# Performance work log

Hardware: AMD Instinct MI355X
Metric: run time of the kernel (lower is better)

The kernel has to match this reference:

```python
import jax, jax.numpy as jnp
import numpy as np

NUM_NODES = 100000
FEAT_DIM = 256
H1 = 256
H2 = 256
NUM_CLASSES = 64
B = 4096
F1 = 25
F2 = 10


def setup_inputs() -> dict:
    key = jax.random.key(0)
    k0, k1, k2, ke, kw1, kw2, kw3 = jax.random.split(key, 7)
    T0 = jax.random.randint(k0, (B,), 0, NUM_NODES)
    T1 = jax.random.randint(k1, (B, F1), 0, NUM_NODES)
    T2 = jax.random.randint(k2, (B * F1, F2), 0, NUM_NODES)
    emb = jax.random.normal(ke, (NUM_NODES, FEAT_DIM), dtype=jnp.float32)
    # nn.Linear(in, out, bias=False) stores weight as [out, in]
    W1 = jax.random.normal(kw1, (H1, 2 * FEAT_DIM), dtype=jnp.float32) * (1.0 / np.sqrt(2 * FEAT_DIM))
    W2 = jax.random.normal(kw2, (H2, 2 * H1), dtype=jnp.float32) * (1.0 / np.sqrt(2 * H1))
    W3 = jax.random.normal(kw3, (NUM_CLASSES, H2), dtype=jnp.float32) * (1.0 / np.sqrt(H2))
    return {"T0": T0, "T1": T1, "T2": T2, "emb": emb, "W1": W1, "W2": W2, "W3": W3}


def reference(T0, T1, T2, emb, W1, W2, W3):
    # hop-0 roots: [B, D]; hop-1 neighbor mean: [B, D]
    feat_0 = emb[T0]
    x = emb[T1].mean(axis=1)
    h0 = jax.nn.relu(jnp.concatenate([feat_0, x], axis=1) @ W1.T)  # [B, H1]
    # dropout is identity in eval mode (p applied only in training)
    # hop-1 nodes with hop-2 neighbor mean: [B*F1, D] each
    feat_1 = emb[T1].reshape(-1, FEAT_DIM)
    x2 = emb[T2].mean(axis=1)  # [B*F1, D]
    h1 = jax.nn.relu(jnp.concatenate([feat_1, x2], axis=1) @ W1.T)  # [B*F1, H1]
    h1 = h1.reshape(B, F1, H1).mean(axis=1)  # [B, H1]
    combined = jnp.concatenate([h0, h1], axis=1)  # [B, 2*H1]
    embedding = jax.nn.relu(combined @ W2.T)  # [B, H2]
    scores = embedding @ W3.T  # [B, C]
    return scores
```

## Files before the change

kernel.cpp:

```cpp
#include <hip/hip_runtime.h>
#include <hip/hip_bf16.h>


typedef __bf16  bf16x8 __attribute__((ext_vector_type(8)));
typedef __bf16  bf16x4 __attribute__((ext_vector_type(4)));
typedef float   f32x4  __attribute__((ext_vector_type(4)));
typedef float   f32x2  __attribute__((ext_vector_type(2)));

#define BATCH     4096
#define F1        25
#define F2        10
#define NNODES    100000
#define ZY_NT     3125
#define ZY_BLOCKS 512

__device__ __forceinline__ uint2 pack4_bf16(float a, float b, float c, float d) {
    union { __bf16 h[4]; uint2 u; } p;
    p.h[0] = (__bf16)a; p.h[1] = (__bf16)b; p.h[2] = (__bf16)c; p.h[3] = (__bf16)d;
    return p.u;
}

__global__ __launch_bounds__(256) void prep_weights(const float* __restrict__ W1,
                                                    const float* __restrict__ W2,
                                                    const float* __restrict__ W3,
                                                    __bf16* __restrict__ Wzy,
                                                    __bf16* __restrict__ W2b,
                                                    __bf16* __restrict__ W3b) {
    int blk = blockIdx.x;
    if (blk < 64) {
        int i = blk * 256 + threadIdx.x;
        int r  = i >> 5;
        int c0 = (i & 31) * 8;
        const float* src = (r < 256) ? (W1 + (size_t)r * 512 + c0)
                                     : (W1 + (size_t)(r - 256) * 512 + 256 + c0);
        float4 a = reinterpret_cast<const float4*>(src)[0];
        float4 b = reinterpret_cast<const float4*>(src)[1];
        uint4 o;
        uint2 pa = pack4_bf16(a.x, a.y, a.z, a.w);
        uint2 pb = pack4_bf16(b.x, b.y, b.z, b.w);
        o.x = pa.x; o.y = pa.y; o.z = pb.x; o.w = pb.y;
        *reinterpret_cast<uint4*>(Wzy + (size_t)r * 256 + c0) = o;
    } else {
        const float* in; __bf16* out;
        int i;
        if (blk < 128) { in = W2; out = W2b; i = (blk - 64) * 256 + threadIdx.x; }
        else           { in = W3; out = W3b; i = (blk - 128) * 256 + threadIdx.x; }
        float4 v0 = reinterpret_cast<const float4*>(in)[i * 2];
        float4 v1 = reinterpret_cast<const float4*>(in)[i * 2 + 1];
        uint4 o;
        uint2 a = pack4_bf16(v0.x, v0.y, v0.z, v0.w);
        uint2 b = pack4_bf16(v1.x, v1.y, v1.z, v1.w);
        o.x = a.x; o.y = a.y; o.z = b.x; o.w = b.y;
        reinterpret_cast<uint4*>(out)[i] = o;
    }
}

__global__ __launch_bounds__(512, 2) void gemm_ZY(const float* __restrict__ emb,
                                                  const __bf16* __restrict__ Wzy,
                                                  __bf16* __restrict__ Ztab,
                                                  unsigned char* __restrict__ Y8) {
    __shared__ __align__(16) char Abuf[2][16384];
    __shared__ __align__(16) __bf16 Ybuf[8][32][72];
    const int tid  = threadIdx.x;
    const int wid  = tid >> 6;
    const int lane = tid & 63;
    const int lr   = lane & 15;
    const int kg   = lane >> 4;
    const int n0   = wid * 64;

    bf16x8 wfrag[4][8];
    {
        const __bf16* Wb = Wzy + (size_t)(n0 + lr) * 256 + kg * 8;
#pragma unroll
        for (int ni = 0; ni < 4; ++ni)
#pragma unroll
            for (int kt = 0; kt < 8; ++kt)
                wfrag[ni][kt] = *reinterpret_cast<const bf16x8*>(Wb + ni * 16 * 256 + kt * 32);
    }

    int soff[4];
#pragma unroll
    for (int q = 0; q < 4; ++q) {
        int e  = q * 2048 + tid * 4;
        int r  = e >> 8;
        int cb = (e & 255) * 2;
        soff[q] = r * 512 + (cb ^ ((r & 7) << 4));
    }

    int t = blockIdx.x;
    float4 ld0[4];
    {
        const float4* src = reinterpret_cast<const float4*>(emb + (size_t)t * 8192);
#pragma unroll
        for (int q = 0; q < 4; ++q) ld0[q] = src[q * 512 + tid];
    }
    int cur = 0;

    for (; t < ZY_NT; t += ZY_BLOCKS) {
#pragma unroll
        for (int q = 0; q < 4; ++q) {
            float4 v = ld0[q];
            *reinterpret_cast<uint2*>(Abuf[cur] + soff[q]) = pack4_bf16(v.x, v.y, v.z, v.w);
        }
        int tn = t + ZY_BLOCKS;
        float4 ld1[4] = {};
        if (tn < ZY_NT) {
            const float4* src = reinterpret_cast<const float4*>(emb + (size_t)tn * 8192);
#pragma unroll
            for (int q = 0; q < 4; ++q) ld1[q] = src[q * 512 + tid];
        }
        __syncthreads();

        f32x4 acc[2][4] = {};
        const char* Ab = Abuf[cur];
#pragma unroll
        for (int kt = 0; kt < 8; ++kt) {
            bf16x8 a[2];
#pragma unroll
            for (int mi = 0; mi < 2; ++mi) {
                int r  = mi * 16 + lr;
                int by = kt * 64 + kg * 16;
                a[mi] = *reinterpret_cast<const bf16x8*>(Ab + r * 512 + (by ^ ((r & 7) << 4)));
            }
#pragma unroll
            for (int mi = 0; mi < 2; ++mi)
#pragma unroll
                for (int ni = 0; ni < 4; ++ni)
                    acc[mi][ni] = __builtin_amdgcn_mfma_f32_16x16x32_bf16(a[mi], wfrag[ni][kt], acc[mi][ni], 0, 0, 0);
        }

        const int orow = (lane >> 4) * 4;
        const int ocol = lane & 15;
        const int m0   = t * 32;
#pragma unroll
        for (int mi = 0; mi < 2; ++mi)
#pragma unroll
            for (int ni = 0; ni < 4; ++ni)
#pragma unroll
                for (int j = 0; j < 4; ++j)
                    Ybuf[wid][mi * 16 + orow + j][ni * 16 + ocol] = (__bf16)acc[mi][ni][j];
        const int row = lane & 31;
        const int cg  = (lane >> 5) * 32;
        if (wid < 4) {
#pragma unroll
            for (int q = 0; q < 4; ++q) {
                bf16x8 v = *reinterpret_cast<bf16x8*>(&Ybuf[wid][row][cg + q * 8]);
                *reinterpret_cast<bf16x8*>(Ztab + (size_t)(m0 + row) * 256 + n0 + cg + q * 8) = v;
            }
        } else {
#pragma unroll
            for (int q = 0; q < 4; ++q) {
                bf16x8 v = *reinterpret_cast<bf16x8*>(&Ybuf[wid][row][cg + q * 8]);
                int w0 = 0, w1 = 0;
                w0 = __builtin_amdgcn_cvt_pk_fp8_f32((float)v[0], (float)v[1], w0, false);
                w0 = __builtin_amdgcn_cvt_pk_fp8_f32((float)v[2], (float)v[3], w0, true);
                w1 = __builtin_amdgcn_cvt_pk_fp8_f32((float)v[4], (float)v[5], w1, false);
                w1 = __builtin_amdgcn_cvt_pk_fp8_f32((float)v[6], (float)v[7], w1, true);
                uint2 o; o.x = (unsigned)w0; o.y = (unsigned)w1;
                *reinterpret_cast<uint2*>(Y8 + (size_t)(m0 + row) * 256 + (n0 - 256) + cg + q * 8) = o;
            }
        }

#pragma unroll
        for (int q = 0; q < 4; ++q) ld0[q] = ld1[q];
        cur ^= 1;
    }
}

__global__ __launch_bounds__(256) void agg_kernel(const int* __restrict__ T0,
                                                  const int* __restrict__ T1,
                                                  const int* __restrict__ T2,
                                                  const __bf16* __restrict__ Ztab,
                                                  const unsigned char* __restrict__ Y8,
                                                  __bf16* __restrict__ comb) {
    __shared__ float red1[4][256];
    __shared__ float red0[4][256];
    const int b    = blockIdx.x;
    const int wv   = threadIdx.x >> 6;
    const int lane = threadIdx.x & 63;
    float macc[4] = {};
    float h0y[4]  = {};

    for (int f = wv; f < F1; f += 4) {
        const int r  = __builtin_amdgcn_readfirstlane(b * F1 + f);
        const int t1 = T1[r];
        int idx[F2];
#pragma unroll
        for (int j = 0; j < F2; ++j) idx[j] = T2[(size_t)r * F2 + j];

        bf16x4 z = *reinterpret_cast<const bf16x4*>(Ztab + (size_t)t1 * 256 + lane * 4);
        unsigned int y1 = *reinterpret_cast<const unsigned int*>(Y8 + (size_t)t1 * 256 + lane * 4);
        float sy[4] = {};
#pragma unroll
        for (int j = 0; j < F2; ++j) {
            unsigned int yv = *reinterpret_cast<const unsigned int*>(Y8 + (size_t)idx[j] * 256 + lane * 4);
            f32x2 lo = __builtin_amdgcn_cvt_pk_f32_fp8(yv, false);
            f32x2 hi = __builtin_amdgcn_cvt_pk_f32_fp8(yv, true);
            sy[0] += lo[0]; sy[1] += lo[1]; sy[2] += hi[0]; sy[3] += hi[1];
        }
        {
            f32x2 lo = __builtin_amdgcn_cvt_pk_f32_fp8(y1, false);
            f32x2 hi = __builtin_amdgcn_cvt_pk_f32_fp8(y1, true);
            h0y[0] += lo[0]; h0y[1] += lo[1]; h0y[2] += hi[0]; h0y[3] += hi[1];
        }
#pragma unroll
        for (int e = 0; e < 4; ++e)
            macc[e] += fmaxf((float)z[e] + sy[e] * (1.0f / F2), 0.0f);
    }

    float4 t1v; t1v.x = macc[0]; t1v.y = macc[1]; t1v.z = macc[2]; t1v.w = macc[3];
    float4 t0v; t0v.x = h0y[0];  t0v.y = h0y[1];  t0v.z = h0y[2];  t0v.w = h0y[3];
    *reinterpret_cast<float4*>(&red1[wv][lane * 4]) = t1v;
    *reinterpret_cast<float4*>(&red0[wv][lane * 4]) = t0v;
    __syncthreads();

    const int col = threadIdx.x;
    float s1 = red1[0][col] + red1[1][col] + red1[2][col] + red1[3][col];
    float s0 = red0[0][col] + red0[1][col] + red0[2][col] + red0[3][col];
    const int t0 = T0[b];
    float z0 = (float)Ztab[(size_t)t0 * 256 + col];
    comb[(size_t)b * 512 + col]       = (__bf16)fmaxf(z0 + s0 * (1.0f / F1), 0.0f);
    comb[(size_t)b * 512 + 256 + col] = (__bf16)(s1 * (1.0f / F1));
}

__global__ __launch_bounds__(256) void gemm_relu_bf16(const __bf16* __restrict__ A,
                                                      const __bf16* __restrict__ W,
                                                      __bf16* __restrict__ C,
                                                      int K, int ldc) {
    int wid  = threadIdx.x >> 6;
    int lane = threadIdx.x & 63;
    int m0 = blockIdx.x * 128 + (wid >> 1) * 64;
    int n0 = blockIdx.y * 128 + (wid & 1) * 64;
    int lr = lane & 15;
    int kg = lane >> 4;

    f32x4 acc[4][4] = {};
    const __bf16* Abase = A + (size_t)(m0 + lr) * K + kg * 8;
    const __bf16* Wbase = W + (size_t)(n0 + lr) * K + kg * 8;

    for (int kt = 0; kt < K; kt += 32) {
        bf16x8 a[4], b[4];
#pragma unroll
        for (int i = 0; i < 4; ++i)
            a[i] = *reinterpret_cast<const bf16x8*>(Abase + (size_t)i * 16 * K + kt);
#pragma unroll
        for (int i = 0; i < 4; ++i)
            b[i] = *reinterpret_cast<const bf16x8*>(Wbase + (size_t)i * 16 * K + kt);
#pragma unroll
        for (int mi = 0; mi < 4; ++mi)
#pragma unroll
            for (int ni = 0; ni < 4; ++ni)
                acc[mi][ni] = __builtin_amdgcn_mfma_f32_16x16x32_bf16(a[mi], b[ni], acc[mi][ni], 0, 0, 0);
    }

    int orow = (lane >> 4) * 4;
    int ocol = lane & 15;
#pragma unroll
    for (int mi = 0; mi < 4; ++mi)
#pragma unroll
        for (int ni = 0; ni < 4; ++ni)
#pragma unroll
            for (int j = 0; j < 4; ++j) {
                float v = fmaxf(acc[mi][ni][j], 0.0f);
                C[(size_t)(m0 + mi * 16 + orow + j) * ldc + (n0 + ni * 16 + ocol)] = (__bf16)v;
            }
}

__global__ __launch_bounds__(256) void gemm_out(const __bf16* __restrict__ A,
                                                const __bf16* __restrict__ W,
                                                float* __restrict__ C) {
    const int K = 256;
    int wid  = threadIdx.x >> 6;
    int lane = threadIdx.x & 63;
    int m0 = blockIdx.x * 128 + wid * 32;
    int lr = lane & 15;
    int kg = lane >> 4;

    f32x4 acc[2][4] = {};
    const __bf16* Abase = A + (size_t)(m0 + lr) * K + kg * 8;
    const __bf16* Wbase = W + (size_t)lr * K + kg * 8;

    for (int kt = 0; kt < K; kt += 32) {
        bf16x8 a[2], b[4];
#pragma unroll
        for (int i = 0; i < 2; ++i)
            a[i] = *reinterpret_cast<const bf16x8*>(Abase + (size_t)i * 16 * K + kt);
#pragma unroll
        for (int i = 0; i < 4; ++i)
            b[i] = *reinterpret_cast<const bf16x8*>(Wbase + (size_t)i * 16 * K + kt);
#pragma unroll
        for (int mi = 0; mi < 2; ++mi)
#pragma unroll
            for (int ni = 0; ni < 4; ++ni)
                acc[mi][ni] = __builtin_amdgcn_mfma_f32_16x16x32_bf16(a[mi], b[ni], acc[mi][ni], 0, 0, 0);
    }

    int orow = (lane >> 4) * 4;
    int ocol = lane & 15;
#pragma unroll
    for (int mi = 0; mi < 2; ++mi)
#pragma unroll
        for (int ni = 0; ni < 4; ++ni)
#pragma unroll
            for (int j = 0; j < 4; ++j)
                C[(size_t)(m0 + mi * 16 + orow + j) * 64 + (ni * 16 + ocol)] = acc[mi][ni][j];
}

extern "C" void kernel_launch(void* const* d_in, const int* in_sizes, int n_in,
                              void* d_out, int out_size, void* d_ws, size_t ws_size,
                              hipStream_t stream) {
    const int*   T0  = (const int*)d_in[0];
    const int*   T1  = (const int*)d_in[1];
    const int*   T2  = (const int*)d_in[2];
    const float* emb = (const float*)d_in[3];
    const float* W1  = (const float*)d_in[4];
    const float* W2  = (const float*)d_in[5];
    const float* W3  = (const float*)d_in[6];
    float* out = (float*)d_out;

    char* ws = (char*)d_ws;
    __bf16*        Wzy  = (__bf16*)(ws);
    __bf16*        W2b  = (__bf16*)(ws + 262144);
    __bf16*        W3b  = (__bf16*)(ws + 524288);
    __bf16*        comb = (__bf16*)(ws + 557056);
    __bf16*        embd = (__bf16*)(ws + 4751360);
    __bf16*        Ztab = (__bf16*)(ws + 6848512);
    unsigned char* Y8   = (unsigned char*)(ws + 58048512);

    prep_weights<<<dim3(136), dim3(256), 0, stream>>>(W1, W2, W3, Wzy, W2b, W3b);

    gemm_ZY<<<dim3(ZY_BLOCKS), dim3(512), 0, stream>>>(emb, Wzy, Ztab, Y8);

    agg_kernel<<<dim3(BATCH), dim3(256), 0, stream>>>(T0, T1, T2, Ztab, Y8, comb);

    gemm_relu_bf16<<<dim3(BATCH / 128, 2), dim3(256), 0, stream>>>(comb, W2b, embd, 512, 256);
    gemm_out<<<dim3(BATCH / 128), dim3(256), 0, stream>>>(embd, W3b, out);
}
```

Baseline: 130.6 us.

## Use atomic tile scheduler in gemm_ZY and store MFMA outputs directly

Replaces the static grid-stride tile loop in gemm_ZY with a dynamic work queue: a global counter, initialised in prep_weights, hands out tiles via atomicAdd, and the next tile index is fetched one iteration ahead with double-buffered shared slots. It also swaps the MFMA operand order so each lane's accumulator holds consecutive output columns. That lets results be packed and written straight to global memory, dropping the shared-memory Ybuf transpose and its LDS traffic. The aim is better load balance across blocks and less LDS use, which may help occupancy. The cost is an atomic per tile and narrower, less coalesced global stores.

```diff
diff --git a/kernel.cpp b/kernel.cpp
--- a/kernel.cpp
+++ b/kernel.cpp
@@ -20,13 +20,22 @@
     return p.u;
 }
 
+__device__ __forceinline__ unsigned int pack4_bf16_u1(float a, float b, float c, float d,
+                                                      unsigned int* hi) {
+    uint2 u = pack4_bf16(a, b, c, d);
+    *hi = u.y;
+    return u.x;
+}
+
 __global__ __launch_bounds__(256) void prep_weights(const float* __restrict__ W1,
                                                     const float* __restrict__ W2,
                                                     const float* __restrict__ W3,
                                                     __bf16* __restrict__ Wzy,
                                                     __bf16* __restrict__ W2b,
-                                                    __bf16* __restrict__ W3b) {
+                                                    __bf16* __restrict__ W3b,
+                                                    int* __restrict__ cnt) {
     int blk = blockIdx.x;
+    if (blk == 0 && threadIdx.x == 0) *cnt = ZY_BLOCKS;
     if (blk < 64) {
         int i = blk * 256 + threadIdx.x;
         int r  = i >> 5;
@@ -58,9 +67,10 @@
 __global__ __launch_bounds__(512, 2) void gemm_ZY(const float* __restrict__ emb,
                                                   const __bf16* __restrict__ Wzy,
                                                   __bf16* __restrict__ Ztab,
-                                                  unsigned char* __restrict__ Y8) {
+                                                  unsigned char* __restrict__ Y8,
+                                                  int* __restrict__ cnt) {
     __shared__ __align__(16) char Abuf[2][16384];
-    __shared__ __align__(16) __bf16 Ybuf[8][32][72];
+    __shared__ int sTile[2];
     const int tid  = threadIdx.x;
     const int wid  = tid >> 6;
     const int lane = tid & 63;
@@ -87,28 +97,31 @@
         soff[q] = r * 512 + (cb ^ ((r & 7) << 4));
     }
 
-    int t = blockIdx.x;
+    int tCur = blockIdx.x;
+    if (tid == 0) sTile[1] = atomicAdd(cnt, 1);
     float4 ld0[4];
     {
-        const float4* src = reinterpret_cast<const float4*>(emb + (size_t)t * 8192);
+        const float4* src = reinterpret_cast<const float4*>(emb + (size_t)tCur * 8192);
 #pragma unroll
         for (int q = 0; q < 4; ++q) ld0[q] = src[q * 512 + tid];
     }
-    int cur = 0;
-
-    for (; t < ZY_NT; t += ZY_BLOCKS) {
+    __syncthreads();
+    int tNext = sTile[1];
+
+    int cur = 0, par = 0;
+    while (tCur < ZY_NT) {
 #pragma unroll
         for (int q = 0; q < 4; ++q) {
             float4 v = ld0[q];
             *reinterpret_cast<uint2*>(Abuf[cur] + soff[q]) = pack4_bf16(v.x, v.y, v.z, v.w);
         }
-        int tn = t + ZY_BLOCKS;
         float4 ld1[4] = {};
-        if (tn < ZY_NT) {
-            const float4* src = reinterpret_cast<const float4*>(emb + (size_t)tn * 8192);
+        if (tNext < ZY_NT) {
+            const float4* src = reinterpret_cast<const float4*>(emb + (size_t)tNext * 8192);
 #pragma unroll
             for (int q = 0; q < 4; ++q) ld1[q] = src[q * 512 + tid];
         }
+        if (tid == 0) sTile[par] = atomicAdd(cnt, 1);
         __syncthreads();
 
         f32x4 acc[2][4] = {};
@@ -126,44 +139,44 @@
             for (int mi = 0; mi < 2; ++mi)
 #pragma unroll
                 for (int ni = 0; ni < 4; ++ni)
-                    acc[mi][ni] = __builtin_amdgcn_mfma_f32_16x16x32_bf16(a[mi], wfrag[ni][kt], acc[mi][ni], 0, 0, 0);
-        }
-
-        const int orow = (lane >> 4) * 4;
-        const int ocol = lane & 15;
-        const int m0   = t * 32;
-#pragma unroll
-        for (int mi = 0; mi < 2; ++mi)
-#pragma unroll
-            for (int ni = 0; ni < 4; ++ni)
-#pragma unroll
-                for (int j = 0; j < 4; ++j)
-                    Ybuf[wid][mi * 16 + orow + j][ni * 16 + ocol] = (__bf16)acc[mi][ni][j];
-        const int row = lane & 31;
-        const int cg  = (lane >> 5) * 32;
-        if (wid < 4) {
-#pragma unroll
-            for (int q = 0; q < 4; ++q) {
-                bf16x8 v = *reinterpret_cast<bf16x8*>(&Ybuf[wid][row][cg + q * 8]);
-                *reinterpret_cast<bf16x8*>(Ztab + (size_t)(m0 + row) * 256 + n0 + cg + q * 8) = v;
+                    acc[mi][ni] = __builtin_amdgcn_mfma_f32_16x16x32_bf16(wfrag[ni][kt], a[mi], acc[mi][ni], 0, 0, 0);
+        }
+
+        {
+            const int m0   = tCur * 32;
+            const int mrow = lane & 15;
+            const int csub = (lane >> 4) * 4;
+            if (wid < 4) {
+#pragma unroll
+                for (int mi = 0; mi < 2; ++mi)
+#pragma unroll
+                    for (int ni = 0; ni < 4; ++ni) {
+                        f32x4 v = acc[mi][ni];
+                        uint2 u = pack4_bf16(v[0], v[1], v[2], v[3]);
+                        *reinterpret_cast<uint2*>(Ztab + (size_t)(m0 + mi * 16 + mrow) * 256
+                                                  + n0 + ni * 16 + csub) = u;
+                    }
+            } else {
+#pragma unroll
+                for (int mi = 0; mi < 2; ++mi)
+#pragma unroll
+                    for (int ni = 0; ni < 4; ++ni) {
+                        f32x4 v = acc[mi][ni];
+                        int w = 0;
+                        w = __builtin_amdgcn_cvt_pk_fp8_f32(v[0], v[1], w, false);
+                        w = __builtin_amdgcn_cvt_pk_fp8_f32(v[2], v[3], w, true);
+                        *reinterpret_cast<unsigned int*>(Y8 + (size_t)(m0 + mi * 16 + mrow) * 256
+                                                         + (n0 - 256) + ni * 16 + csub) = (unsigned)w;
+                    }
             }
-        } else {
-#pragma unroll
-            for (int q = 0; q < 4; ++q) {
-                bf16x8 v = *reinterpret_cast<bf16x8*>(&Ybuf[wid][row][cg + q * 8]);
-                int w0 = 0, w1 = 0;
-                w0 = __builtin_amdgcn_cvt_pk_fp8_f32((float)v[0], (float)v[1], w0, false);
-                w0 = __builtin_amdgcn_cvt_pk_fp8_f32((float)v[2], (float)v[3], w0, true);
-                w1 = __builtin_amdgcn_cvt_pk_fp8_f32((float)v[4], (float)v[5], w1, false);
-                w1 = __builtin_amdgcn_cvt_pk_fp8_f32((float)v[6], (float)v[7], w1, true);
-                uint2 o; o.x = (unsigned)w0; o.y = (unsigned)w1;
-                *reinterpret_cast<uint2*>(Y8 + (size_t)(m0 + row) * 256 + (n0 - 256) + cg + q * 8) = o;
-            }
         }
 
 #pragma unroll
         for (int q = 0; q < 4; ++q) ld0[q] = ld1[q];
+        tCur = tNext;
+        tNext = sTile[par];
         cur ^= 1;
+        par ^= 1;
     }
 }
 
@@ -326,10 +339,11 @@
     __bf16*        embd = (__bf16*)(ws + 4751360);
     __bf16*        Ztab = (__bf16*)(ws + 6848512);
     unsigned char* Y8   = (unsigned char*)(ws + 58048512);
-
-    prep_weights<<<dim3(136), dim3(256), 0, stream>>>(W1, W2, W3, Wzy, W2b, W3b);
-
-    gemm_ZY<<<dim3(ZY_BLOCKS), dim3(512), 0, stream>>>(emb, Wzy, Ztab, Y8);
+    int*           cnt  = (int*)(ws + 83648512);
+
+    prep_weights<<<dim3(136), dim3(256), 0, stream>>>(W1, W2, W3, Wzy, W2b, W3b, cnt);
+
+    gemm_ZY<<<dim3(ZY_BLOCKS), dim3(512), 0, stream>>>(emb, Wzy, Ztab, Y8, cnt);
 
     agg_kernel<<<dim3(BATCH), dim3(256), 0, stream>>>(T0, T1, T2, Ztab, Y8, comb);
 
```

Result: slower. 138.7 us (+6.2%).
